# Performance work log

Hardware: AMD Instinct MI355X
Metric: run time of the kernel (lower is better)

The kernel has to match this reference:

```python
import jax, jax.numpy as jnp
import numpy as np

B = 16384   # batch
F = 26      # categorical fields
N = 100000  # rows per embedding table
M = 16      # embedding dim per field
NUM = 13    # numerical (dense) features
D = F * M + NUM  # embed_output_dim = 429
L = 6       # CrossNet layers (vector parameterization)
H = 1024    # MLP hidden


def setup_inputs() -> dict:
    key = jax.random.key(0)
    ks = jax.random.split(key, 10)
    Xi = jax.random.randint(ks[0], (B, F, 1), 0, N)
    Xv = jax.random.normal(ks[1], (B, NUM), dtype=jnp.float32)
    # per-field tables, init U(-sqrt(1/n), sqrt(1/n)) as in the torch code; stacked flat
    bound = float(np.sqrt(1.0 / N))
    emb_tables = jax.random.uniform(ks[2], (F * N, M), jnp.float32, -bound, bound)
    cross_w = jax.random.normal(ks[3], (L, D), dtype=jnp.float32) * 0.02
    cross_b = jnp.zeros((L, D), dtype=jnp.float32)
    W1 = jax.random.normal(ks[4], (D, H), dtype=jnp.float32) * (1.0 / np.sqrt(D))
    b1 = jnp.zeros((H,), dtype=jnp.float32)
    W2 = jax.random.normal(ks[5], (H, H), dtype=jnp.float32) * (1.0 / np.sqrt(H))
    b2 = jnp.zeros((H,), dtype=jnp.float32)
    Wout = jax.random.normal(ks[6], (H + D, 1), dtype=jnp.float32) * (1.0 / np.sqrt(H + D))
    bout = jnp.zeros((1,), dtype=jnp.float32)
    return dict(Xi=Xi, Xv=Xv, emb_tables=emb_tables, cross_w=cross_w,
                cross_b=cross_b, W1=W1, b1=b1, W2=W2, b2=b2, Wout=Wout, bout=bout)


def reference(Xi, Xv, emb_tables, cross_w, cross_b, W1, b1, W2, b2, Wout, bout):
    # Fused multi-table EmbeddingBag(mode='sum'): one gather over the stacked tables.
    offs = (jnp.arange(F, dtype=Xi.dtype) * N)[None, :, None]        # [1,F,1]
    flat_idx = (Xi + offs).reshape(-1)                               # [B*F*K]
    g = emb_tables[flat_idx].reshape(B, F, -1, M).sum(axis=2)        # [B,F,M] bag-sum
    x0 = jnp.concatenate([Xv, g.reshape(B, F * M)], axis=1)          # [B,D]
    # CrossNet, vector parameterization: x_{l+1} = x0 * (x_l . w_l) + b_l + x_l
    x = x0
    for l in range(L):
        xw = x @ cross_w[l]                                          # [B]
        x = x0 * xw[:, None] + cross_b[l] + x
    # Deep MLP on x0
    h = jax.nn.relu(x0 @ W1 + b1)
    h = jax.nn.relu(h @ W2 + b2)
    out = jnp.concatenate([h, x], axis=1) @ Wout + bout              # [B,1]
    return out[:, 0]
```

## Files before the change

kernel.cpp:

```cpp
#include <hip/hip_runtime.h>
#include <hip/hip_bf16.h>

#define B_   16384
#define F_   26
#define N_   100000
#define M_   16
#define NUM_ 13
#define D_   429
#define KP1_ 448
#define L_   6
#define H_   1024

typedef unsigned short u16;
typedef __bf16 bf16x8 __attribute__((ext_vector_type(8)));
typedef float  f32x4  __attribute__((ext_vector_type(4)));

__device__ __forceinline__ u16 f2bf_bits(float f) {
  union { float f; unsigned u; } x; x.f = f;
  unsigned r = x.u + 0x7FFFu + ((x.u >> 16) & 1u);
  return (u16)(r >> 16);
}

__global__ __launch_bounds__(256) void build_cross(
    const int* __restrict__ Xi, const float* __restrict__ Xv,
    const float* __restrict__ emb,
    const float* __restrict__ cw, const float* __restrict__ cb,
    const float* __restrict__ Wout, const float* __restrict__ bout,
    u16* __restrict__ x0b, float* __restrict__ out) {
  __shared__ u16 sbuf[4][KP1_];
  const int w = threadIdx.x >> 6, lane = threadIdx.x & 63;
  const int b = blockIdx.x * 4 + w;
  const int* xi = Xi + b * F_;

  float x0r[7];
  #pragma unroll
  for (int i = 0; i < 7; ++i) {
    int e = i * 64 + lane;
    float v = 0.f;
    if (e < 416) {
      int f = e >> 4;
      int idx = xi[f];
      v = emb[((size_t)f * N_ + idx) * M_ + (e & 15)];
    } else if (e < D_) {
      v = Xv[b * NUM_ + (e - 416)];
    }
    x0r[i] = v;
    sbuf[w][e] = f2bf_bits(v);
  }

  float xr[7];
  #pragma unroll
  for (int i = 0; i < 7; ++i) xr[i] = x0r[i];
  for (int l = 0; l < L_; ++l) {
    float wl[7], bl[7];
    #pragma unroll
    for (int i = 0; i < 7; ++i) {
      int e = i * 64 + lane;
      if (e < D_) {
        int d = (e < 416) ? (13 + e) : (e - 416);
        wl[i] = cw[l * D_ + d]; bl[i] = cb[l * D_ + d];
      } else { wl[i] = 0.f; bl[i] = 0.f; }
    }
    float s = 0.f;
    #pragma unroll
    for (int i = 0; i < 7; ++i) s += xr[i] * wl[i];
    #pragma unroll
    for (int off = 32; off; off >>= 1) s += __shfl_xor(s, off);
    #pragma unroll
    for (int i = 0; i < 7; ++i) xr[i] = x0r[i] * s + bl[i] + xr[i];
  }

  __syncthreads();
  if (lane < 56)
    ((uint4*)(x0b + (size_t)b * KP1_))[lane] = ((const uint4*)sbuf[w])[lane];

  float s = 0.f;
  #pragma unroll
  for (int i = 0; i < 7; ++i) {
    int e = i * 64 + lane;
    if (e < D_) {
      int d = (e < 416) ? (13 + e) : (e - 416);
      s += xr[i] * Wout[H_ + d];
    }
  }
  #pragma unroll
  for (int off = 32; off; off >>= 1) s += __shfl_xor(s, off);
  if (lane == 0) out[b] = s + bout[0];
}

__global__ void prep_w(const float* __restrict__ W1, const float* __restrict__ W2,
                       u16* __restrict__ w1bt, u16* __restrict__ w2bt) {
  int t = blockIdx.x * blockDim.x + threadIdx.x;
  if (t < H_ * KP1_) {
    int n = t / KP1_, e = t % KP1_;
    float v = 0.f;
    if (e < D_) {
      int d = (e < 416) ? (13 + e) : (e - 416);
      v = W1[(size_t)d * H_ + n];
    }
    w1bt[t] = f2bf_bits(v);
  } else {
    int t2 = t - H_ * KP1_;
    if (t2 < H_ * H_) {
      int n = t2 / H_, k = t2 % H_;
      w2bt[t2] = f2bf_bits(W2[(size_t)k * H_ + n]);
    }
  }
}

template<int MODE>
__global__ __launch_bounds__(512, 2) void gemm256(
    const u16* __restrict__ A, const u16* __restrict__ BT,
    const float* __restrict__ bias, u16* __restrict__ C,
    const float* __restrict__ Wout, float* __restrict__ out,
    int N, int K) {
  __shared__ __align__(16) u16 As[4][256 * 32];
  __shared__ __align__(16) u16 Bs[4][256 * 32];
  const int nbx = N >> 8;
  const int bx = blockIdx.x % nbx;
  const int by = blockIdx.x / nbx;
  const int tid = threadIdx.x;
  const int w = tid >> 6, l = tid & 63;
  const int wr = w >> 2, wc = w & 3;
  const int nkt = K >> 5;

  const int srow = l >> 2;
  const int schunk = (l & 3) ^ ((l >> 3) & 3);
  const u16* gA = A  + (size_t)(by * 256 + w * 16 + srow) * K + schunk * 8;
  const u16* gB = BT + (size_t)(bx * 256 + w * 16 + srow) * K + schunk * 8;
  const int ldsoff = w * 16 * 32;

  auto stage = [&](int t) {
    const int buf = t & 3;
    const u16* a = gA + t * 32;
    const u16* b = gB + t * 32;
    #pragma unroll
    for (int i = 0; i < 2; ++i)
      __builtin_amdgcn_global_load_lds(
          (const __attribute__((address_space(1))) void*)(a + (size_t)i * 128 * K),
          (__attribute__((address_space(3))) void*)&As[buf][ldsoff + i * 128 * 32], 16, 0, 0);
    #pragma unroll
    for (int i = 0; i < 2; ++i)
      __builtin_amdgcn_global_load_lds(
          (const __attribute__((address_space(1))) void*)(b + (size_t)i * 128 * K),
          (__attribute__((address_space(3))) void*)&Bs[buf][ldsoff + i * 128 * 32], 16, 0, 0);
  };

  stage(0); stage(1); stage(2);

  const int fr = l & 15;
  const int fs = ((l >> 4) ^ ((fr >> 1) & 3)) << 4;
  const int aoff = (wr * 128 + fr) * 64 + fs;
  const int boff = (wc * 64 + fr) * 64 + fs;

  f32x4 acc[8][4] = {};

  asm volatile("s_waitcnt vmcnt(8)" ::: "memory");
  __builtin_amdgcn_s_barrier();

  for (int t = 0; t < nkt; ++t) {
    if (t + 3 < nkt) stage(t + 3);
    const char* Ab = (const char*)&As[t & 3][0];
    const char* Bb = (const char*)&Bs[t & 3][0];
    bf16x8 af[8], bf[4];
    #pragma unroll
    for (int m = 0; m < 8; ++m) af[m] = *(const bf16x8*)(Ab + aoff + m * 1024);
    #pragma unroll
    for (int n = 0; n < 4; ++n) bf[n] = *(const bf16x8*)(Bb + boff + n * 1024);
    __builtin_amdgcn_s_setprio(1);
    #pragma unroll
    for (int m = 0; m < 8; ++m)
      #pragma unroll
      for (int n = 0; n < 4; ++n)
        acc[m][n] = __builtin_amdgcn_mfma_f32_16x16x32_bf16(af[m], bf[n], acc[m][n], 0, 0, 0);
    __builtin_amdgcn_s_setprio(0);
    if (t + 3 < nkt)      asm volatile("s_waitcnt vmcnt(8)" ::: "memory");
    else if (t + 2 < nkt) asm volatile("s_waitcnt vmcnt(4)" ::: "memory");
    else if (t + 1 < nkt) asm volatile("s_waitcnt vmcnt(0)" ::: "memory");
    if (t + 1 < nkt) __builtin_amdgcn_s_barrier();
  }

  const int g4 = l >> 4;
  const int ccol0 = bx * 256 + wc * 64;
  const int row0 = by * 256 + wr * 128 + g4 * 4;
  if (MODE == 0) {
    #pragma unroll
    for (int n = 0; n < 4; ++n) {
      int col = ccol0 + n * 16 + fr;
      float bv = bias[col];
      #pragma unroll
      for (int m = 0; m < 8; ++m)
        #pragma unroll
        for (int r = 0; r < 4; ++r) {
          float v = fmaxf(acc[m][n][r] + bv, 0.f);
          C[(size_t)(row0 + m * 16 + r) * N + col] = f2bf_bits(v);
        }
    }
  } else {
    float bv[4], wv[4];
    #pragma unroll
    for (int n = 0; n < 4; ++n) {
      int col = ccol0 + n * 16 + fr;
      bv[n] = bias[col]; wv[n] = Wout[col];
    }
    #pragma unroll
    for (int m = 0; m < 8; ++m)
      #pragma unroll
      for (int r = 0; r < 4; ++r) {
        float s = 0.f;
        #pragma unroll
        for (int n = 0; n < 4; ++n) {
          float v = fmaxf(acc[m][n][r] + bv[n], 0.f);
          s = fmaf(v, wv[n], s);
        }
        s += __shfl_xor(s, 1); s += __shfl_xor(s, 2);
        s += __shfl_xor(s, 4); s += __shfl_xor(s, 8);
        if (fr == 0) atomicAdd(out + row0 + m * 16 + r, s);
      }
  }
}

extern "C" void kernel_launch(void* const* d_in, const int* in_sizes, int n_in,
                              void* d_out, int out_size, void* d_ws, size_t ws_size,
                              hipStream_t stream) {
  const int*   Xi   = (const int*)d_in[0];
  const float* Xv   = (const float*)d_in[1];
  const float* emb  = (const float*)d_in[2];
  const float* cw   = (const float*)d_in[3];
  const float* cb   = (const float*)d_in[4];
  const float* W1   = (const float*)d_in[5];
  const float* b1   = (const float*)d_in[6];
  const float* W2   = (const float*)d_in[7];
  const float* b2   = (const float*)d_in[8];
  const float* Wout = (const float*)d_in[9];
  const float* bout = (const float*)d_in[10];
  float* out = (float*)d_out;

  char* ws = (char*)d_ws;
  size_t off = 0;
  auto alloc = [&](size_t bytes) {
    void* p = ws + off; off += (bytes + 255) & ~(size_t)255; return p;
  };
  u16* x0b  = (u16*)alloc((size_t)B_ * KP1_ * 2);
  u16* w1bt = (u16*)alloc((size_t)H_ * KP1_ * 2);
  u16* w2bt = (u16*)alloc((size_t)H_ * H_ * 2);
  u16* h1   = (u16*)alloc((size_t)B_ * H_ * 2);

  hipLaunchKernelGGL(build_cross, dim3(B_ / 4), dim3(256), 0, stream,
                     Xi, Xv, emb, cw, cb, Wout, bout, x0b, out);
  hipLaunchKernelGGL(prep_w, dim3((H_ * KP1_ + H_ * H_ + 255) / 256), dim3(256), 0, stream,
                     W1, W2, w1bt, w2bt);
  hipLaunchKernelGGL((gemm256<0>), dim3((B_ / 256) * (H_ / 256)), dim3(512), 0, stream,
                     x0b, w1bt, b1, h1, nullptr, nullptr, H_, KP1_);
  hipLaunchKernelGGL((gemm256<1>), dim3((B_ / 256) * (H_ / 256)), dim3(512), 0, stream,
                     h1, w2bt, b2, nullptr, Wout, out, H_, H_);
}
```

Measured before the change: 114.1 us.

## Fuse cross and weight-prep kernels, swizzle GEMM blocks, double-buffer LDS fragments

```diff
diff --git a/kernel.cpp b/kernel.cpp
--- a/kernel.cpp
+++ b/kernel.cpp
@@ -21,89 +21,91 @@
   return (u16)(r >> 16);
 }
 
-__global__ __launch_bounds__(256) void build_cross(
+__global__ __launch_bounds__(256) void fused_front(
     const int* __restrict__ Xi, const float* __restrict__ Xv,
     const float* __restrict__ emb,
     const float* __restrict__ cw, const float* __restrict__ cb,
     const float* __restrict__ Wout, const float* __restrict__ bout,
-    u16* __restrict__ x0b, float* __restrict__ out) {
+    const float* __restrict__ W1, const float* __restrict__ W2,
+    u16* __restrict__ x0b, u16* __restrict__ w1bt, u16* __restrict__ w2bt,
+    float* __restrict__ out) {
   __shared__ u16 sbuf[4][KP1_];
-  const int w = threadIdx.x >> 6, lane = threadIdx.x & 63;
-  const int b = blockIdx.x * 4 + w;
-  const int* xi = Xi + b * F_;
-
-  float x0r[7];
-  #pragma unroll
-  for (int i = 0; i < 7; ++i) {
-    int e = i * 64 + lane;
-    float v = 0.f;
-    if (e < 416) {
-      int f = e >> 4;
-      int idx = xi[f];
-      v = emb[((size_t)f * N_ + idx) * M_ + (e & 15)];
-    } else if (e < D_) {
-      v = Xv[b * NUM_ + (e - 416)];
-    }
-    x0r[i] = v;
-    sbuf[w][e] = f2bf_bits(v);
-  }
-
-  float xr[7];
-  #pragma unroll
-  for (int i = 0; i < 7; ++i) xr[i] = x0r[i];
-  for (int l = 0; l < L_; ++l) {
-    float wl[7], bl[7];
+  const int blk = blockIdx.x;
+  if (blk < B_ / 4) {
+    const int w = threadIdx.x >> 6, lane = threadIdx.x & 63;
+    const int b = blk * 4 + w;
+    const int* xi = Xi + b * F_;
+
+    float x0r[7];
+    #pragma unroll
+    for (int i = 0; i < 7; ++i) {
+      int e = i * 64 + lane;
+      float v = 0.f;
+      if (e < 416) {
+        int f = e >> 4;
+        int idx = xi[f];
+        v = emb[((size_t)f * N_ + idx) * M_ + (e & 15)];
+      } else if (e < D_) {
+        v = Xv[b * NUM_ + (e - 416)];
+      }
+      x0r[i] = v;
+      sbuf[w][e] = f2bf_bits(v);
+    }
+
+    float xr[7];
+    #pragma unroll
+    for (int i = 0; i < 7; ++i) xr[i] = x0r[i];
+    for (int l = 0; l < L_; ++l) {
+      float wl[7], bl[7];
+      #pragma unroll
+      for (int i = 0; i < 7; ++i) {
+        int e = i * 64 + lane;
+        if (e < D_) {
+          int d = (e < 416) ? (13 + e) : (e - 416);
+          wl[i] = cw[l * D_ + d]; bl[i] = cb[l * D_ + d];
+        } else { wl[i] = 0.f; bl[i] = 0.f; }
+      }
+      float s = 0.f;
+      #pragma unroll
+      for (int i = 0; i < 7; ++i) s += xr[i] * wl[i];
+      #pragma unroll
+      for (int off = 32; off; off >>= 1) s += __shfl_xor(s, off);
+      #pragma unroll
+      for (int i = 0; i < 7; ++i) xr[i] = x0r[i] * s + bl[i] + xr[i];
+    }
+
+    __syncthreads();
+    if (lane < 56)
+      ((uint4*)(x0b + (size_t)b * KP1_))[lane] = ((const uint4*)sbuf[w])[lane];
+
+    float s = 0.f;
     #pragma unroll
     for (int i = 0; i < 7; ++i) {
       int e = i * 64 + lane;
       if (e < D_) {
         int d = (e < 416) ? (13 + e) : (e - 416);
-        wl[i] = cw[l * D_ + d]; bl[i] = cb[l * D_ + d];
-      } else { wl[i] = 0.f; bl[i] = 0.f; }
-    }
-    float s = 0.f;
-    #pragma unroll
-    for (int i = 0; i < 7; ++i) s += xr[i] * wl[i];
+        s += xr[i] * Wout[H_ + d];
+      }
+    }
     #pragma unroll
     for (int off = 32; off; off >>= 1) s += __shfl_xor(s, off);
-    #pragma unroll
-    for (int i = 0; i < 7; ++i) xr[i] = x0r[i] * s + bl[i] + xr[i];
-  }
-
-  __syncthreads();
-  if (lane < 56)
-    ((uint4*)(x0b + (size_t)b * KP1_))[lane] = ((const uint4*)sbuf[w])[lane];
-
-  float s = 0.f;
-  #pragma unroll
-  for (int i = 0; i < 7; ++i) {
-    int e = i * 64 + lane;
-    if (e < D_) {
-      int d = (e < 416) ? (13 + e) : (e - 416);
-      s += xr[i] * Wout[H_ + d];
-    }
-  }
-  #pragma unroll
-  for (int off = 32; off; off >>= 1) s += __shfl_xor(s, off);
-  if (lane == 0) out[b] = s + bout[0];
-}
-
-__global__ void prep_w(const float* __restrict__ W1, const float* __restrict__ W2,
-                       u16* __restrict__ w1bt, u16* __restrict__ w2bt) {
-  int t = blockIdx.x * blockDim.x + threadIdx.x;
-  if (t < H_ * KP1_) {
-    int n = t / KP1_, e = t % KP1_;
-    float v = 0.f;
-    if (e < D_) {
-      int d = (e < 416) ? (13 + e) : (e - 416);
-      v = W1[(size_t)d * H_ + n];
-    }
-    w1bt[t] = f2bf_bits(v);
+    if (lane == 0) out[b] = s + bout[0];
   } else {
-    int t2 = t - H_ * KP1_;
-    if (t2 < H_ * H_) {
-      int n = t2 / H_, k = t2 % H_;
-      w2bt[t2] = f2bf_bits(W2[(size_t)k * H_ + n]);
+    int t = (blk - B_ / 4) * 256 + threadIdx.x;
+    if (t < H_ * KP1_) {
+      int n = t / KP1_, e = t % KP1_;
+      float v = 0.f;
+      if (e < D_) {
+        int d = (e < 416) ? (13 + e) : (e - 416);
+        v = W1[(size_t)d * H_ + n];
+      }
+      w1bt[t] = f2bf_bits(v);
+    } else {
+      int t2 = t - H_ * KP1_;
+      if (t2 < H_ * H_) {
+        int n = t2 / H_, k = t2 % H_;
+        w2bt[t2] = f2bf_bits(W2[(size_t)k * H_ + n]);
+      }
     }
   }
 }
@@ -117,8 +119,10 @@
   __shared__ __align__(16) u16 As[4][256 * 32];
   __shared__ __align__(16) u16 Bs[4][256 * 32];
   const int nbx = N >> 8;
-  const int bx = blockIdx.x % nbx;
-  const int by = blockIdx.x / nbx;
+  const int cpx = gridDim.x >> 3;
+  const int swz = (blockIdx.x & 7) * cpx + (blockIdx.x >> 3);
+  const int bx = swz % nbx;
+  const int by = swz / nbx;
   const int tid = threadIdx.x;
   const int w = tid >> 6, l = tid & 63;
   const int wr = w >> 2, wc = w & 3;
@@ -146,27 +150,22 @@
           (__attribute__((address_space(3))) void*)&Bs[buf][ldsoff + i * 128 * 32], 16, 0, 0);
   };
 
-  stage(0); stage(1); stage(2);
-
   const int fr = l & 15;
   const int fs = ((l >> 4) ^ ((fr >> 1) & 3)) << 4;
   const int aoff = (wr * 128 + fr) * 64 + fs;
   const int boff = (wc * 64 + fr) * 64 + fs;
 
+  auto read_frags = [&](int tt, bf16x8 (&af)[8], bf16x8 (&bf)[4]) {
+    const char* Ab = (const char*)&As[tt & 3][0];
+    const char* Bb = (const char*)&Bs[tt & 3][0];
+    #pragma unroll
+    for (int m = 0; m < 8; ++m) af[m] = *(const bf16x8*)(Ab + aoff + m * 1024);
+    #pragma unroll
+    for (int n = 0; n < 4; ++n) bf[n] = *(const bf16x8*)(Bb + boff + n * 1024);
+  };
+
   f32x4 acc[8][4] = {};
-
-  asm volatile("s_waitcnt vmcnt(8)" ::: "memory");
-  __builtin_amdgcn_s_barrier();
-
-  for (int t = 0; t < nkt; ++t) {
-    if (t + 3 < nkt) stage(t + 3);
-    const char* Ab = (const char*)&As[t & 3][0];
-    const char* Bb = (const char*)&Bs[t & 3][0];
-    bf16x8 af[8], bf[4];
-    #pragma unroll
-    for (int m = 0; m < 8; ++m) af[m] = *(const bf16x8*)(Ab + aoff + m * 1024);
-    #pragma unroll
-    for (int n = 0; n < 4; ++n) bf[n] = *(const bf16x8*)(Bb + boff + n * 1024);
+  auto mfma_all = [&](bf16x8 (&af)[8], bf16x8 (&bf)[4]) {
     __builtin_amdgcn_s_setprio(1);
     #pragma unroll
     for (int m = 0; m < 8; ++m)
@@ -174,10 +173,34 @@
       for (int n = 0; n < 4; ++n)
         acc[m][n] = __builtin_amdgcn_mfma_f32_16x16x32_bf16(af[m], bf[n], acc[m][n], 0, 0, 0);
     __builtin_amdgcn_s_setprio(0);
-    if (t + 3 < nkt)      asm volatile("s_waitcnt vmcnt(8)" ::: "memory");
-    else if (t + 2 < nkt) asm volatile("s_waitcnt vmcnt(4)" ::: "memory");
-    else if (t + 1 < nkt) asm volatile("s_waitcnt vmcnt(0)" ::: "memory");
-    if (t + 1 < nkt) __builtin_amdgcn_s_barrier();
+  };
+
+  stage(0); stage(1); stage(2);
+  asm volatile("s_waitcnt vmcnt(4)" ::: "memory");
+  __builtin_amdgcn_s_barrier();
+  bf16x8 afA[8], bfA[4], afB[8], bfB[4];
+  read_frags(0, afA, bfA);
+
+  for (int t = 0; t < nkt; t += 2) {
+    if (t + 3 < nkt) stage(t + 3);
+    if (t + 1 < nkt) read_frags(t + 1, afB, bfB);
+    mfma_all(afA, bfA);
+    if (t + 2 < nkt) {
+      if (t + 3 < nkt) asm volatile("s_waitcnt vmcnt(4)" ::: "memory");
+      else             asm volatile("s_waitcnt vmcnt(0)" ::: "memory");
+      __builtin_amdgcn_s_barrier();
+    }
+    const int u = t + 1;
+    if (u < nkt) {
+      if (u + 3 < nkt) stage(u + 3);
+      if (u + 1 < nkt) read_frags(u + 1, afA, bfA);
+      mfma_all(afB, bfB);
+      if (u + 2 < nkt) {
+        if (u + 3 < nkt) asm volatile("s_waitcnt vmcnt(4)" ::: "memory");
+        else             asm volatile("s_waitcnt vmcnt(0)" ::: "memory");
+        __builtin_amdgcn_s_barrier();
+      }
+    }
   }
 
   const int g4 = l >> 4;
@@ -246,10 +269,9 @@
   u16* w2bt = (u16*)alloc((size_t)H_ * H_ * 2);
   u16* h1   = (u16*)alloc((size_t)B_ * H_ * 2);
 
-  hipLaunchKernelGGL(build_cross, dim3(B_ / 4), dim3(256), 0, stream,
-                     Xi, Xv, emb, cw, cb, Wout, bout, x0b, out);
-  hipLaunchKernelGGL(prep_w, dim3((H_ * KP1_ + H_ * H_ + 255) / 256), dim3(256), 0, stream,
-                     W1, W2, w1bt, w2bt);
+  const int prep_blocks = (H_ * KP1_ + H_ * H_) / 256;
+  hipLaunchKernelGGL(fused_front, dim3(B_ / 4 + prep_blocks), dim3(256), 0, stream,
+                     Xi, Xv, emb, cw, cb, Wout, bout, W1, W2, x0b, w1bt, w2bt, out);
   hipLaunchKernelGGL((gemm256<0>), dim3((B_ / 256) * (H_ / 256)), dim3(512), 0, stream,
                      x0b, w1bt, b1, h1, nullptr, nullptr, H_, KP1_);
   hipLaunchKernelGGL((gemm256<1>), dim3((B_ / 256) * (H_ / 256)), dim3(512), 0, stream,
```

Result: faster. 107.2 us (-6.0%).
